# Kernel tuning notes

Measured on AMD Instinct MI355X. Metric: run time of the kernel, lower is better.

Reference implementation:

```python
import jax, jax.numpy as jnp
import numpy as np
from functools import partial

T = 16  # number of ODE time steps (h = 1/T)


def _q(x0, xt, t):
    """Nadaraya-Watson Gaussian RBF retrieval.
    x0: (B, d) memory bank, xt: (N, d) queries, t: scalar time.
    Returns qt: (N, d).
    Original torch code subtracts the *global* min of zz before exp;
    that constant cancels in the row-wise normalization, so this is
    exactly a softmax over the bank dimension of -0.5*||z||^2.
    """
    sigma_t = t
    alpha_t = 1.0 - t
    # (N, B, d) diff tensor -- the dominant memory traffic
    z = (xt[:, None, :] - alpha_t * x0[None, :, :]) / sigma_t
    zz = jnp.sum(z * z, axis=-1)                 # (N, B)
    wt = jax.nn.softmax(-0.5 * zz, axis=-1)      # (N, B)
    return wt @ x0                               # (N, d)


def _G(x0, xt, t):
    return (xt - _q(x0, xt, t)) / t


def setup_inputs() -> dict:
    key = jax.random.key(0)
    k1, k2 = jax.random.split(key)
    x1 = jax.random.normal(k1, (2048, 8), dtype=jnp.float32)   # (N, d) Gaussian states at t=1
    x0 = jax.random.normal(k2, (4096, 8), dtype=jnp.float32)   # (B, d) memory bank / data batch
    return {"x1": x1, "x0": x0}


def reference(x1, x0):
    h = 1.0 / T
    G1 = _G(x0, x1, 1.0)
    # Heun (trapezoidal predictor-corrector) integration from t=1 down to t=h.
    # t after step i (0-based) is 1 - h*(i+1); always > 0 for i < T-1.
    t_vals = 1.0 - h * (jnp.arange(1, T, dtype=jnp.float32))   # (T-1,)

    def step(carry, t):
        xt, G1 = carry
        G2 = _G(x0, xt - G1 * h, t)
        xt = xt - (G1 + G2) * (h * 0.5)
        return (xt, G2), None

    (xt, _), _ = jax.lax.scan(step, (x1, G1), t_vals)
    return xt  # (N, d)
```

## Files before the change

### kernel.cpp

```cpp
#include <hip/hip_runtime.h>


#define NQ     2048
#define NB     4096
#define TSTEPS 16
#define BLOCK  512

#if defined(__has_builtin)
#if __has_builtin(__builtin_amdgcn_exp2f)
#define EXP2(x) __builtin_amdgcn_exp2f(x)
#endif
#endif
#ifndef EXP2
#define EXP2(x) exp2f(x)
#endif

__device__ __forceinline__ void eval_pair(
        const float4* __restrict__ lds_lo,
        const float4* __restrict__ lds_hi,
        float (*mrg)[2][12],
        const float (&xq)[2][8], float t, int lane, int h, int w,
        float (&Gout)[2][8])
{
    const float c0      = -0.72134752044448170f / (t * t);
    const float alpha   = 1.0f - t;
    const float thr_off = 40.0f / c0;
    float mz[2] = {3.0e38f, 3.0e38f};
    float th[2] = {3.0e38f, 3.0e38f};
    float t0[2] = {0.0f, 0.0f};
    float s[2]  = {0.0f, 0.0f};
    float q[2][8];
#pragma unroll
    for (int qq = 0; qq < 2; ++qq)
#pragma unroll
        for (int j = 0; j < 8; ++j) q[qq][j] = 0.0f;

    const int b0 = lane + h * 2048;

#pragma unroll 2
    for (int g = 0; g < 8; ++g) {
        float4 lo[4], hi[4];
        float  zz[2][4];
#pragma unroll
        for (int e = 0; e < 4; ++e) {
            const int b = b0 + g * 256 + e * 64;
            lo[e] = lds_lo[b];
            hi[e] = lds_hi[b];
#pragma unroll
            for (int qq = 0; qq < 2; ++qq) {
                float z, acc;
                z = fmaf(-alpha, lo[e].x, xq[qq][0]); acc = z * z;
                z = fmaf(-alpha, lo[e].y, xq[qq][1]); acc = fmaf(z, z, acc);
                z = fmaf(-alpha, lo[e].z, xq[qq][2]); acc = fmaf(z, z, acc);
                z = fmaf(-alpha, lo[e].w, xq[qq][3]); acc = fmaf(z, z, acc);
                z = fmaf(-alpha, hi[e].x, xq[qq][4]); acc = fmaf(z, z, acc);
                z = fmaf(-alpha, hi[e].y, xq[qq][5]); acc = fmaf(z, z, acc);
                z = fmaf(-alpha, hi[e].z, xq[qq][6]); acc = fmaf(z, z, acc);
                z = fmaf(-alpha, hi[e].w, xq[qq][7]); acc = fmaf(z, z, acc);
                zz[qq][e] = acc;
            }
        }
#pragma unroll
        for (int qq = 0; qq < 2; ++qq) {
            const float bz = fminf(fminf(zz[qq][0], zz[qq][1]),
                                   fminf(zz[qq][2], zz[qq][3]));
            if (__any(bz < th[qq])) {
                const float mzn = fminf(mz[qq], bz);
                const float c = EXP2(c0 * (mz[qq] - mzn));
                s[qq] *= c;
#pragma unroll
                for (int j = 0; j < 8; ++j) q[qq][j] *= c;
                mz[qq] = mzn;
                th[qq] = mzn + thr_off;
                t0[qq] = -c0 * mzn;
            }
#pragma unroll
            for (int e = 0; e < 4; ++e) {
                const float wgt = EXP2(fmaf(c0, zz[qq][e], t0[qq]));
                s[qq] += wgt;
                q[qq][0] = fmaf(wgt, lo[e].x, q[qq][0]);
                q[qq][1] = fmaf(wgt, lo[e].y, q[qq][1]);
                q[qq][2] = fmaf(wgt, lo[e].z, q[qq][2]);
                q[qq][3] = fmaf(wgt, lo[e].w, q[qq][3]);
                q[qq][4] = fmaf(wgt, hi[e].x, q[qq][4]);
                q[qq][5] = fmaf(wgt, hi[e].y, q[qq][5]);
                q[qq][6] = fmaf(wgt, hi[e].z, q[qq][6]);
                q[qq][7] = fmaf(wgt, hi[e].w, q[qq][7]);
            }
        }
    }

#pragma unroll
    for (int qq = 0; qq < 2; ++qq) {
        float mw = mz[qq];
#pragma unroll
        for (int off = 32; off >= 1; off >>= 1)
            mw = fminf(mw, __shfl_xor(mw, off));
        const float c = EXP2(c0 * (mz[qq] - mw));
        s[qq] *= c;
#pragma unroll
        for (int j = 0; j < 8; ++j) q[qq][j] *= c;
        mz[qq] = mw;
#pragma unroll
        for (int off = 32; off >= 1; off >>= 1) {
            s[qq] += __shfl_xor(s[qq], off);
#pragma unroll
            for (int j = 0; j < 8; ++j) q[qq][j] += __shfl_xor(q[qq][j], off);
        }
    }

    if (lane == 0) {
#pragma unroll
        for (int qq = 0; qq < 2; ++qq) {
            float* p = mrg[w][qq];
            p[0] = mz[qq];
            p[1] = s[qq];
#pragma unroll
            for (int j = 0; j < 8; ++j) p[2 + j] = q[qq][j];
        }
    }
    __syncthreads();
    const int pw = w ^ 1;
    const float invT = 1.0f / t;
#pragma unroll
    for (int qq = 0; qq < 2; ++qq) {
        const float* p = mrg[pw][qq];
        const float mzb = p[0], sb = p[1];
        const float M  = fminf(mz[qq], mzb);
        const float ca = EXP2(c0 * (mz[qq] - M));
        const float cb = EXP2(c0 * (mzb  - M));
        const float S  = ca * s[qq] + cb * sb;
        const float invS = 1.0f / S;
#pragma unroll
        for (int j = 0; j < 8; ++j) {
            const float Q = ca * q[qq][j] + cb * p[2 + j];
            Gout[qq][j] = fmaf(-Q, invS, xq[qq][j]) * invT;
        }
    }
    __syncthreads();
}

__global__ __launch_bounds__(BLOCK, 2) void flow_ode_kernel(
        const float* __restrict__ x1,
        const float* __restrict__ x0,
        float* __restrict__ out)
{
    __shared__ float4 lds_lo[NB];
    __shared__ float4 lds_hi[NB];
    __shared__ float  mrg[8][2][12];

    const int tid  = threadIdx.x;
    const int w    = tid >> 6;
    const int lane = tid & 63;

    float sm[8];
#pragma unroll
    for (int j = 0; j < 8; ++j) sm[j] = 0.0f;
#pragma unroll
    for (int i = 0; i < NB / BLOCK; ++i) {
        const int b = tid + i * BLOCK;
        const float4* p = reinterpret_cast<const float4*>(x0) + 2 * b;
        const float4 lo = p[0], hi = p[1];
        lds_lo[b] = lo;
        lds_hi[b] = hi;
        sm[0] += lo.x; sm[1] += lo.y; sm[2] += lo.z; sm[3] += lo.w;
        sm[4] += hi.x; sm[5] += hi.y; sm[6] += hi.z; sm[7] += hi.w;
    }
#pragma unroll
    for (int off = 32; off >= 1; off >>= 1)
#pragma unroll
        for (int j = 0; j < 8; ++j) sm[j] += __shfl_xor(sm[j], off);
    if (lane == 0) {
#pragma unroll
        for (int j = 0; j < 8; ++j) mrg[w][0][j] = sm[j];
    }
    __syncthreads();
    float mean[8];
#pragma unroll
    for (int j = 0; j < 8; ++j) {
        float acc = 0.0f;
#pragma unroll
        for (int wv = 0; wv < 8; ++wv) acc += mrg[wv][0][j];
        mean[j] = acc * (1.0f / (float)NB);
    }
    __syncthreads();

    const int h     = w & 1;
    const int pair  = w >> 1;
    const int qbase = blockIdx.x * 8 + pair * 2;

    float xt[2][8], G1[2][8];
#pragma unroll
    for (int qq = 0; qq < 2; ++qq) {
        const float4* p = reinterpret_cast<const float4*>(x1) + 2 * (qbase + qq);
        const float4 a = p[0], b4 = p[1];
        xt[qq][0] = a.x;  xt[qq][1] = a.y;  xt[qq][2] = a.z;  xt[qq][3] = a.w;
        xt[qq][4] = b4.x; xt[qq][5] = b4.y; xt[qq][6] = b4.z; xt[qq][7] = b4.w;
    }
#pragma unroll
    for (int qq = 0; qq < 2; ++qq)
#pragma unroll
        for (int j = 0; j < 8; ++j) G1[qq][j] = xt[qq][j] - mean[j];

    const float hstep = 0.0625f;
    for (int i = 1; i < TSTEPS; ++i) {
        const float t = 1.0f - hstep * (float)i;
        float xe[2][8], G2[2][8];
#pragma unroll
        for (int qq = 0; qq < 2; ++qq)
#pragma unroll
            for (int j = 0; j < 8; ++j)
                xe[qq][j] = fmaf(-hstep, G1[qq][j], xt[qq][j]);
        eval_pair(lds_lo, lds_hi, mrg, xe, t, lane, h, w, G2);
#pragma unroll
        for (int qq = 0; qq < 2; ++qq)
#pragma unroll
            for (int j = 0; j < 8; ++j) {
                xt[qq][j] = fmaf(-0.03125f, G1[qq][j] + G2[qq][j], xt[qq][j]);
                G1[qq][j] = G2[qq][j];
            }
    }

    if (h == 0 && lane == 0) {
#pragma unroll
        for (int qq = 0; qq < 2; ++qq) {
            float4 a, b4;
            a.x  = xt[qq][0]; a.y  = xt[qq][1]; a.z  = xt[qq][2]; a.w  = xt[qq][3];
            b4.x = xt[qq][4]; b4.y = xt[qq][5]; b4.z = xt[qq][6]; b4.w = xt[qq][7];
            float4* o = reinterpret_cast<float4*>(out + (qbase + qq) * 8);
            o[0] = a;
            o[1] = b4;
        }
    }
}

extern "C" void kernel_launch(void* const* d_in, const int* in_sizes, int n_in,
                              void* d_out, int out_size, void* d_ws, size_t ws_size,
                              hipStream_t stream) {
    const float* x1 = (const float*)d_in[0];
    const float* x0 = (const float*)d_in[1];
    float* out = (float*)d_out;

    flow_ode_kernel<<<NQ / 8, BLOCK, 0, stream>>>(x1, x0, out);
}
```

Measured before the change: 185.9 us.

## Split each query pair across four waves with 1024-thread blocks

Doubles the block to 16 waves. Each pair of queries is now handled by four waves, each scanning a quarter of the memory bank instead of a half. The cross-wave merge now combines four partial softmax states (min, sum, weighted sum) instead of two. The goal is to double resident waves per CU, since LDS capacity already limits residency to one block per CU, and so hide exp and LDS latency better. The cost is more merge work per step and tighter per-thread register limits under the new launch bounds.

```diff
diff --git a/kernel.cpp b/kernel.cpp
--- a/kernel.cpp
+++ b/kernel.cpp
@@ -4,7 +4,8 @@
 #define NQ     2048
 #define NB     4096
 #define TSTEPS 16
-#define BLOCK  512
+#define BLOCK  1024
+#define NWAVE  16
 
 #if defined(__has_builtin)
 #if __has_builtin(__builtin_amdgcn_exp2f)
@@ -19,7 +20,7 @@
         const float4* __restrict__ lds_lo,
         const float4* __restrict__ lds_hi,
         float (*mrg)[2][12],
-        const float (&xq)[2][8], float t, int lane, int h, int w,
+        const float (&xq)[2][8], float t, int lane, int quad, int w,
         float (&Gout)[2][8])
 {
     const float c0      = -0.72134752044448170f / (t * t);
@@ -35,10 +36,10 @@
 #pragma unroll
         for (int j = 0; j < 8; ++j) q[qq][j] = 0.0f;
 
-    const int b0 = lane + h * 2048;
-
-#pragma unroll 2
-    for (int g = 0; g < 8; ++g) {
+    const int b0 = lane + quad * 1024;
+
+#pragma unroll
+    for (int g = 0; g < 4; ++g) {
         float4 lo[4], hi[4];
         float  zz[2][4];
 #pragma unroll
@@ -120,34 +121,45 @@
         }
     }
     __syncthreads();
-    const int pw = w ^ 1;
+    const int g0 = w & ~3;
     const float invT = 1.0f / t;
 #pragma unroll
     for (int qq = 0; qq < 2; ++qq) {
-        const float* p = mrg[pw][qq];
-        const float mzb = p[0], sb = p[1];
-        const float M  = fminf(mz[qq], mzb);
-        const float ca = EXP2(c0 * (mz[qq] - M));
-        const float cb = EXP2(c0 * (mzb  - M));
-        const float S  = ca * s[qq] + cb * sb;
+        float mzk[4], sk[4];
+#pragma unroll
+        for (int k = 0; k < 4; ++k) {
+            mzk[k] = mrg[g0 + k][qq][0];
+            sk[k]  = mrg[g0 + k][qq][1];
+        }
+        const float M = fminf(fminf(mzk[0], mzk[1]), fminf(mzk[2], mzk[3]));
+        float ck[4];
+        float S = 0.0f;
+#pragma unroll
+        for (int k = 0; k < 4; ++k) {
+            ck[k] = EXP2(c0 * (mzk[k] - M));
+            S = fmaf(ck[k], sk[k], S);
+        }
         const float invS = 1.0f / S;
 #pragma unroll
         for (int j = 0; j < 8; ++j) {
-            const float Q = ca * q[qq][j] + cb * p[2 + j];
+            float Q = 0.0f;
+#pragma unroll
+            for (int k = 0; k < 4; ++k)
+                Q = fmaf(ck[k], mrg[g0 + k][qq][2 + j], Q);
             Gout[qq][j] = fmaf(-Q, invS, xq[qq][j]) * invT;
         }
     }
     __syncthreads();
 }
 
-__global__ __launch_bounds__(BLOCK, 2) void flow_ode_kernel(
+__global__ __launch_bounds__(BLOCK, 4) void flow_ode_kernel(
         const float* __restrict__ x1,
         const float* __restrict__ x0,
         float* __restrict__ out)
 {
     __shared__ float4 lds_lo[NB];
     __shared__ float4 lds_hi[NB];
-    __shared__ float  mrg[8][2][12];
+    __shared__ float  mrg[NWAVE][2][12];
 
     const int tid  = threadIdx.x;
     const int w    = tid >> 6;
@@ -180,14 +192,14 @@
     for (int j = 0; j < 8; ++j) {
         float acc = 0.0f;
 #pragma unroll
-        for (int wv = 0; wv < 8; ++wv) acc += mrg[wv][0][j];
+        for (int wv = 0; wv < NWAVE; ++wv) acc += mrg[wv][0][j];
         mean[j] = acc * (1.0f / (float)NB);
     }
     __syncthreads();
 
-    const int h     = w & 1;
-    const int pair  = w >> 1;
-    const int qbase = blockIdx.x * 8 + pair * 2;
+    const int quad  = w & 3;
+    const int grp   = w >> 2;
+    const int qbase = blockIdx.x * 8 + grp * 2;
 
     float xt[2][8], G1[2][8];
 #pragma unroll
@@ -211,7 +223,7 @@
 #pragma unroll
             for (int j = 0; j < 8; ++j)
                 xe[qq][j] = fmaf(-hstep, G1[qq][j], xt[qq][j]);
-        eval_pair(lds_lo, lds_hi, mrg, xe, t, lane, h, w, G2);
+        eval_pair(lds_lo, lds_hi, mrg, xe, t, lane, quad, w, G2);
 #pragma unroll
         for (int qq = 0; qq < 2; ++qq)
 #pragma unroll
@@ -221,7 +233,7 @@
             }
     }
 
-    if (h == 0 && lane == 0) {
+    if (quad == 0 && lane == 0) {
 #pragma unroll
         for (int qq = 0; qq < 2; ++qq) {
             float4 a, b4;
```

Measured after the change: 305.9 us. 64.6% more time.

## Process one query per wave pair with 1024-thread blocks

Applied to the files above, without the earlier changes.

Each wave now handles a single query instead of two, and the block grows to 16 waves so a block still covers 8 queries. The grid size and per-block LDS copy of the bank are unchanged. This halves per-wave register state and fully unrolls the bank loop, giving more waves per CU to hide LDS and exp latency. In exchange each bank element read from LDS now feeds only one query, doubling LDS traffic per unit of work, and the larger block makes the per-step barriers costlier.

```diff
diff --git a/kernel.cpp b/kernel.cpp
--- a/kernel.cpp
+++ b/kernel.cpp
@@ -4,7 +4,8 @@
 #define NQ     2048
 #define NB     4096
 #define TSTEPS 16
-#define BLOCK  512
+#define BLOCK  1024
+#define NWAVE  16
 
 #if defined(__has_builtin)
 #if __has_builtin(__builtin_amdgcn_exp2f)
@@ -15,139 +16,120 @@
 #define EXP2(x) exp2f(x)
 #endif
 
-__device__ __forceinline__ void eval_pair(
+__device__ __forceinline__ void eval_one(
         const float4* __restrict__ lds_lo,
         const float4* __restrict__ lds_hi,
-        float (*mrg)[2][12],
-        const float (&xq)[2][8], float t, int lane, int h, int w,
-        float (&Gout)[2][8])
+        float (*mrg)[12],
+        const float (&xq)[8], float t, int lane, int h, int w,
+        float (&Gout)[8])
 {
     const float c0      = -0.72134752044448170f / (t * t);
     const float alpha   = 1.0f - t;
     const float thr_off = 40.0f / c0;
-    float mz[2] = {3.0e38f, 3.0e38f};
-    float th[2] = {3.0e38f, 3.0e38f};
-    float t0[2] = {0.0f, 0.0f};
-    float s[2]  = {0.0f, 0.0f};
-    float q[2][8];
-#pragma unroll
-    for (int qq = 0; qq < 2; ++qq)
-#pragma unroll
-        for (int j = 0; j < 8; ++j) q[qq][j] = 0.0f;
+    float mz = 3.0e38f;
+    float th = 3.0e38f;
+    float t0 = 0.0f;
+    float s  = 0.0f;
+    float q[8];
+#pragma unroll
+    for (int j = 0; j < 8; ++j) q[j] = 0.0f;
 
     const int b0 = lane + h * 2048;
 
-#pragma unroll 2
+#pragma unroll
     for (int g = 0; g < 8; ++g) {
         float4 lo[4], hi[4];
-        float  zz[2][4];
+        float  zz[4];
 #pragma unroll
         for (int e = 0; e < 4; ++e) {
             const int b = b0 + g * 256 + e * 64;
             lo[e] = lds_lo[b];
             hi[e] = lds_hi[b];
-#pragma unroll
-            for (int qq = 0; qq < 2; ++qq) {
-                float z, acc;
-                z = fmaf(-alpha, lo[e].x, xq[qq][0]); acc = z * z;
-                z = fmaf(-alpha, lo[e].y, xq[qq][1]); acc = fmaf(z, z, acc);
-                z = fmaf(-alpha, lo[e].z, xq[qq][2]); acc = fmaf(z, z, acc);
-                z = fmaf(-alpha, lo[e].w, xq[qq][3]); acc = fmaf(z, z, acc);
-                z = fmaf(-alpha, hi[e].x, xq[qq][4]); acc = fmaf(z, z, acc);
-                z = fmaf(-alpha, hi[e].y, xq[qq][5]); acc = fmaf(z, z, acc);
-                z = fmaf(-alpha, hi[e].z, xq[qq][6]); acc = fmaf(z, z, acc);
-                z = fmaf(-alpha, hi[e].w, xq[qq][7]); acc = fmaf(z, z, acc);
-                zz[qq][e] = acc;
-            }
-        }
-#pragma unroll
-        for (int qq = 0; qq < 2; ++qq) {
-            const float bz = fminf(fminf(zz[qq][0], zz[qq][1]),
-                                   fminf(zz[qq][2], zz[qq][3]));
-            if (__any(bz < th[qq])) {
-                const float mzn = fminf(mz[qq], bz);
-                const float c = EXP2(c0 * (mz[qq] - mzn));
-                s[qq] *= c;
-#pragma unroll
-                for (int j = 0; j < 8; ++j) q[qq][j] *= c;
-                mz[qq] = mzn;
-                th[qq] = mzn + thr_off;
-                t0[qq] = -c0 * mzn;
-            }
-#pragma unroll
-            for (int e = 0; e < 4; ++e) {
-                const float wgt = EXP2(fmaf(c0, zz[qq][e], t0[qq]));
-                s[qq] += wgt;
-                q[qq][0] = fmaf(wgt, lo[e].x, q[qq][0]);
-                q[qq][1] = fmaf(wgt, lo[e].y, q[qq][1]);
-                q[qq][2] = fmaf(wgt, lo[e].z, q[qq][2]);
-                q[qq][3] = fmaf(wgt, lo[e].w, q[qq][3]);
-                q[qq][4] = fmaf(wgt, hi[e].x, q[qq][4]);
-                q[qq][5] = fmaf(wgt, hi[e].y, q[qq][5]);
-                q[qq][6] = fmaf(wgt, hi[e].z, q[qq][6]);
-                q[qq][7] = fmaf(wgt, hi[e].w, q[qq][7]);
-            }
-        }
-    }
-
-#pragma unroll
-    for (int qq = 0; qq < 2; ++qq) {
-        float mw = mz[qq];
-#pragma unroll
-        for (int off = 32; off >= 1; off >>= 1)
-            mw = fminf(mw, __shfl_xor(mw, off));
-        const float c = EXP2(c0 * (mz[qq] - mw));
-        s[qq] *= c;
-#pragma unroll
-        for (int j = 0; j < 8; ++j) q[qq][j] *= c;
-        mz[qq] = mw;
-#pragma unroll
-        for (int off = 32; off >= 1; off >>= 1) {
-            s[qq] += __shfl_xor(s[qq], off);
-#pragma unroll
-            for (int j = 0; j < 8; ++j) q[qq][j] += __shfl_xor(q[qq][j], off);
-        }
+            float z, acc;
+            z = fmaf(-alpha, lo[e].x, xq[0]); acc = z * z;
+            z = fmaf(-alpha, lo[e].y, xq[1]); acc = fmaf(z, z, acc);
+            z = fmaf(-alpha, lo[e].z, xq[2]); acc = fmaf(z, z, acc);
+            z = fmaf(-alpha, lo[e].w, xq[3]); acc = fmaf(z, z, acc);
+            z = fmaf(-alpha, hi[e].x, xq[4]); acc = fmaf(z, z, acc);
+            z = fmaf(-alpha, hi[e].y, xq[5]); acc = fmaf(z, z, acc);
+            z = fmaf(-alpha, hi[e].z, xq[6]); acc = fmaf(z, z, acc);
+            z = fmaf(-alpha, hi[e].w, xq[7]); acc = fmaf(z, z, acc);
+            zz[e] = acc;
+        }
+        const float bz = fminf(fminf(zz[0], zz[1]), fminf(zz[2], zz[3]));
+        if (__any(bz < th)) {
+            const float mzn = fminf(mz, bz);
+            const float c = EXP2(c0 * (mz - mzn));
+            s *= c;
+#pragma unroll
+            for (int j = 0; j < 8; ++j) q[j] *= c;
+            mz = mzn;
+            th = mzn + thr_off;
+            t0 = -c0 * mzn;
+        }
+#pragma unroll
+        for (int e = 0; e < 4; ++e) {
+            const float wgt = EXP2(fmaf(c0, zz[e], t0));
+            s += wgt;
+            q[0] = fmaf(wgt, lo[e].x, q[0]);
+            q[1] = fmaf(wgt, lo[e].y, q[1]);
+            q[2] = fmaf(wgt, lo[e].z, q[2]);
+            q[3] = fmaf(wgt, lo[e].w, q[3]);
+            q[4] = fmaf(wgt, hi[e].x, q[4]);
+            q[5] = fmaf(wgt, hi[e].y, q[5]);
+            q[6] = fmaf(wgt, hi[e].z, q[6]);
+            q[7] = fmaf(wgt, hi[e].w, q[7]);
+        }
+    }
+
+    float mw = mz;
+#pragma unroll
+    for (int off = 32; off >= 1; off >>= 1)
+        mw = fminf(mw, __shfl_xor(mw, off));
+    const float cw = EXP2(c0 * (mz - mw));
+    s *= cw;
+#pragma unroll
+    for (int j = 0; j < 8; ++j) q[j] *= cw;
+    mz = mw;
+#pragma unroll
+    for (int off = 32; off >= 1; off >>= 1) {
+        s += __shfl_xor(s, off);
+#pragma unroll
+        for (int j = 0; j < 8; ++j) q[j] += __shfl_xor(q[j], off);
     }
 
     if (lane == 0) {
-#pragma unroll
-        for (int qq = 0; qq < 2; ++qq) {
-            float* p = mrg[w][qq];
-            p[0] = mz[qq];
-            p[1] = s[qq];
-#pragma unroll
-            for (int j = 0; j < 8; ++j) p[2 + j] = q[qq][j];
-        }
-    }
-    __syncthreads();
-    const int pw = w ^ 1;
+        float* p = mrg[w];
+        p[0] = mz;
+        p[1] = s;
+#pragma unroll
+        for (int j = 0; j < 8; ++j) p[2 + j] = q[j];
+    }
+    __syncthreads();
+    const float* p = mrg[w ^ 1];
+    const float mzb = p[0], sb = p[1];
+    const float M    = fminf(mz, mzb);
+    const float ca   = EXP2(c0 * (mz  - M));
+    const float cb   = EXP2(c0 * (mzb - M));
+    const float S    = ca * s + cb * sb;
+    const float invS = 1.0f / S;
     const float invT = 1.0f / t;
 #pragma unroll
-    for (int qq = 0; qq < 2; ++qq) {
-        const float* p = mrg[pw][qq];
-        const float mzb = p[0], sb = p[1];
-        const float M  = fminf(mz[qq], mzb);
-        const float ca = EXP2(c0 * (mz[qq] - M));
-        const float cb = EXP2(c0 * (mzb  - M));
-        const float S  = ca * s[qq] + cb * sb;
-        const float invS = 1.0f / S;
-#pragma unroll
-        for (int j = 0; j < 8; ++j) {
-            const float Q = ca * q[qq][j] + cb * p[2 + j];
-            Gout[qq][j] = fmaf(-Q, invS, xq[qq][j]) * invT;
-        }
+    for (int j = 0; j < 8; ++j) {
+        const float Q = ca * q[j] + cb * p[2 + j];
+        Gout[j] = fmaf(-Q, invS, xq[j]) * invT;
     }
     __syncthreads();
 }
 
-__global__ __launch_bounds__(BLOCK, 2) void flow_ode_kernel(
+__global__ __launch_bounds__(BLOCK) void flow_ode_kernel(
         const float* __restrict__ x1,
         const float* __restrict__ x0,
         float* __restrict__ out)
 {
     __shared__ float4 lds_lo[NB];
     __shared__ float4 lds_hi[NB];
-    __shared__ float  mrg[8][2][12];
+    __shared__ float  mrg[NWAVE][12];
 
     const int tid  = threadIdx.x;
     const int w    = tid >> 6;
@@ -172,7 +154,7 @@
         for (int j = 0; j < 8; ++j) sm[j] += __shfl_xor(sm[j], off);
     if (lane == 0) {
 #pragma unroll
-        for (int j = 0; j < 8; ++j) mrg[w][0][j] = sm[j];
+        for (int j = 0; j < 8; ++j) mrg[w][j] = sm[j];
     }
     __syncthreads();
     float mean[8];
@@ -180,57 +162,46 @@
     for (int j = 0; j < 8; ++j) {
         float acc = 0.0f;
 #pragma unroll
-        for (int wv = 0; wv < 8; ++wv) acc += mrg[wv][0][j];
+        for (int wv = 0; wv < NWAVE; ++wv) acc += mrg[wv][j];
         mean[j] = acc * (1.0f / (float)NB);
     }
     __syncthreads();
 
-    const int h     = w & 1;
-    const int pair  = w >> 1;
-    const int qbase = blockIdx.x * 8 + pair * 2;
-
-    float xt[2][8], G1[2][8];
-#pragma unroll
-    for (int qq = 0; qq < 2; ++qq) {
-        const float4* p = reinterpret_cast<const float4*>(x1) + 2 * (qbase + qq);
+    const int h    = w & 1;
+    const int qidx = blockIdx.x * 8 + (w >> 1);
+
+    float xt[8], G1[8];
+    {
+        const float4* p = reinterpret_cast<const float4*>(x1) + 2 * qidx;
         const float4 a = p[0], b4 = p[1];
-        xt[qq][0] = a.x;  xt[qq][1] = a.y;  xt[qq][2] = a.z;  xt[qq][3] = a.w;
-        xt[qq][4] = b4.x; xt[qq][5] = b4.y; xt[qq][6] = b4.z; xt[qq][7] = b4.w;
-    }
-#pragma unroll
-    for (int qq = 0; qq < 2; ++qq)
-#pragma unroll
-        for (int j = 0; j < 8; ++j) G1[qq][j] = xt[qq][j] - mean[j];
+        xt[0] = a.x;  xt[1] = a.y;  xt[2] = a.z;  xt[3] = a.w;
+        xt[4] = b4.x; xt[5] = b4.y; xt[6] = b4.z; xt[7] = b4.w;
+    }
+#pragma unroll
+    for (int j = 0; j < 8; ++j) G1[j] = xt[j] - mean[j];
 
     const float hstep = 0.0625f;
     for (int i = 1; i < TSTEPS; ++i) {
         const float t = 1.0f - hstep * (float)i;
-        float xe[2][8], G2[2][8];
-#pragma unroll
-        for (int qq = 0; qq < 2; ++qq)
-#pragma unroll
-            for (int j = 0; j < 8; ++j)
-                xe[qq][j] = fmaf(-hstep, G1[qq][j], xt[qq][j]);
-        eval_pair(lds_lo, lds_hi, mrg, xe, t, lane, h, w, G2);
-#pragma unroll
-        for (int qq = 0; qq < 2; ++qq)
-#pragma unroll
-            for (int j = 0; j < 8; ++j) {
-                xt[qq][j] = fmaf(-0.03125f, G1[qq][j] + G2[qq][j], xt[qq][j]);
-                G1[qq][j] = G2[qq][j];
-            }
+        float xe[8], G2[8];
+#pragma unroll
+        for (int j = 0; j < 8; ++j)
+            xe[j] = fmaf(-hstep, G1[j], xt[j]);
+        eval_one(lds_lo, lds_hi, mrg, xe, t, lane, h, w, G2);
+#pragma unroll
+        for (int j = 0; j < 8; ++j) {
+            xt[j] = fmaf(-0.03125f, G1[j] + G2[j], xt[j]);
+            G1[j] = G2[j];
+        }
     }
 
     if (h == 0 && lane == 0) {
-#pragma unroll
-        for (int qq = 0; qq < 2; ++qq) {
-            float4 a, b4;
-            a.x  = xt[qq][0]; a.y  = xt[qq][1]; a.z  = xt[qq][2]; a.w  = xt[qq][3];
-            b4.x = xt[qq][4]; b4.y = xt[qq][5]; b4.z = xt[qq][6]; b4.w = xt[qq][7];
-            float4* o = reinterpret_cast<float4*>(out + (qbase + qq) * 8);
-            o[0] = a;
-            o[1] = b4;
-        }
+        float4 a, b4;
+        a.x  = xt[0]; a.y  = xt[1]; a.z  = xt[2]; a.w  = xt[3];
+        b4.x = xt[4]; b4.y = xt[5]; b4.z = xt[6]; b4.w = xt[7];
+        float4* o = reinterpret_cast<float4*>(out + qidx * 8);
+        o[0] = a;
+        o[1] = b4;
     }
 }
 
```

After: 176.5 us. 1.05x faster.
